# Performance work log

Hardware: AMD Instinct MI355X
Metric: run time of the kernel (lower is better)

The kernel has to match this reference:

```python
import jax, jax.numpy as jnp
import numpy as np

N = 4096
NUM_FEATURES = 1870
HIDDEN = 256
EMBED = 16
ALPHA = 0.2
NEG_BIG = -9e15
EPS = 1e-12


def setup_inputs() -> dict:
    key = jax.random.key(0)
    ks = jax.random.split(key, 9)
    x = jax.random.normal(ks[0], (N, NUM_FEATURES), dtype=jnp.float32)
    # sparse-ish binary adjacency mask (avg degree ~ 41) with self loops
    adj = (jax.random.uniform(ks[1], (N, N)) < 0.01).astype(jnp.float32)
    adj = jnp.maximum(adj, jnp.eye(N, dtype=jnp.float32))
    M = jax.random.uniform(ks[2], (N, N), dtype=jnp.float32)
    s1 = 1.0 / np.sqrt(NUM_FEATURES)
    s2 = 1.0 / np.sqrt(HIDDEN)
    W1 = jax.random.normal(ks[3], (NUM_FEATURES, HIDDEN), dtype=jnp.float32) * s1
    a_self1 = jax.random.normal(ks[4], (HIDDEN, 1), dtype=jnp.float32) * s2
    a_neighs1 = jax.random.normal(ks[5], (HIDDEN, 1), dtype=jnp.float32) * s2
    W2 = jax.random.normal(ks[6], (HIDDEN, EMBED), dtype=jnp.float32) * s2
    a_self2 = jax.random.normal(ks[7], (EMBED, 1), dtype=jnp.float32) / np.sqrt(EMBED)
    a_neighs2 = jax.random.normal(ks[8], (EMBED, 1), dtype=jnp.float32) / np.sqrt(EMBED)
    return {"x": x, "adj": adj, "M": M, "W1": W1, "a_self1": a_self1,
            "a_neighs1": a_neighs1, "W2": W2, "a_self2": a_self2, "a_neighs2": a_neighs2}


def gat_layer(x, adj, M, W, a_self, a_neighs, alpha):
    h = x @ W                                  # [N, out]
    f_self = h @ a_self                        # [N, 1]
    f_neigh = h @ a_neighs                     # [N, 1]
    e = jax.nn.leaky_relu((f_self + f_neigh.T) * M, negative_slope=alpha)  # [N, N]
    e = jnp.where(adj > 0, e, NEG_BIG)
    att = jax.nn.softmax(e, axis=1)            # row-stochastic over neighbors
    return jax.nn.elu(att @ h)                 # [N, out]


def reference(x, adj, M, W1, a_self1, a_neighs1, W2, a_self2, a_neighs2):
    h = gat_layer(x, adj, M, W1, a_self1, a_neighs1, ALPHA)
    h = gat_layer(h, adj, M, W2, a_self2, a_neighs2, ALPHA)
    # F.normalize(h, p=2, dim=1): divide by max(norm, eps)
    norm = jnp.maximum(jnp.linalg.norm(h, axis=1, keepdims=True), EPS)
    z = h / norm                               # [N, EMBED]
    A_pred = jax.nn.sigmoid(z @ z.T)           # [N, N]
    return (A_pred, z)
```

## Files before the change

kernel.cpp:

```cpp
#include <hip/hip_runtime.h>
#include <math.h>

#define NN 4096
#define NFEAT 1870
#define KPAD 2048
#define KSPLIT 8
#define KCHUNK 256
#define HID 256
#define EMB 16
#define MAXDEG 128

typedef __attribute__((ext_vector_type(8))) _Float16 f16x8;
typedef __attribute__((ext_vector_type(4))) float f32x4;

__device__ __forceinline__ ushort f2h(float f) {
    _Float16 h = (_Float16)f;
    return __builtin_bit_cast(ushort, h);
}

__global__ __launch_bounds__(256) void prep_kernel(
    const float* __restrict__ x, ushort* __restrict__ xf,
    const float* __restrict__ W1, ushort* __restrict__ Wh,
    const float* __restrict__ adj, const float* __restrict__ Mmat,
    int* __restrict__ nnz, int* __restrict__ gidx, float* __restrict__ Mg)
{
    const int b = blockIdx.x;
    const int tid = threadIdx.x;
    if (b < NN) {
        const int row = b;
        const int c0 = tid * 8;
        float v[8];
        if (c0 + 8 <= NFEAT) {
#pragma unroll
            for (int j = 0; j < 4; ++j) {
                float2 t = *(const float2*)&x[(size_t)row * NFEAT + c0 + j * 2];
                v[j * 2] = t.x; v[j * 2 + 1] = t.y;
            }
        } else {
#pragma unroll
            for (int j = 0; j < 8; ++j)
                v[j] = (c0 + j < NFEAT) ? x[(size_t)row * NFEAT + c0 + j] : 0.f;
        }
        ushort u[8];
#pragma unroll
        for (int j = 0; j < 8; ++j) u[j] = f2h(v[j]);
        *(int4*)&xf[(size_t)row * KPAD + c0] = *(int4*)u;
    } else if (b < NN + 128) {
        __shared__ float t[64][65];
        const int bb = b - NN;
        const int k0 = (bb & 31) * 64, n0 = (bb >> 5) * 64;
        const int kk = tid >> 2, c4 = (tid & 3) * 16;
#pragma unroll
        for (int j = 0; j < 4; ++j) {
            int k = k0 + kk;
            float4 v = make_float4(0.f, 0.f, 0.f, 0.f);
            if (k < NFEAT) v = *(const float4*)&W1[(size_t)k * HID + n0 + c4 + j * 4];
            t[kk][c4 + j * 4 + 0] = v.x; t[kk][c4 + j * 4 + 1] = v.y;
            t[kk][c4 + j * 4 + 2] = v.z; t[kk][c4 + j * 4 + 3] = v.w;
        }
        __syncthreads();
        const int on = tid >> 2, ok4 = (tid & 3) * 16;
#pragma unroll
        for (int j = 0; j < 4; ++j) {
            ushort hh[4];
#pragma unroll
            for (int i = 0; i < 4; ++i)
                hh[i] = f2h(t[ok4 + j * 4 + i][on]);
            size_t o = (size_t)(n0 + on) * KPAD + k0 + ok4 + j * 4;
            *(ushort4*)&Wh[o] = *(ushort4*)hh;
        }
    } else {
        __shared__ int sidx[4][MAXDEG];
        const int bb = b - NN - 128;
        const int wv = tid >> 6, lane = tid & 63;
        const int row = bb * 4 + wv;
        int base = 0;
#pragma unroll 4
        for (int t4 = 0; t4 < 16; ++t4) {
            int j0 = t4 * 256 + lane * 4;
            float4 a = *(const float4*)&adj[(size_t)row * NN + j0];
            float av[4] = {a.x, a.y, a.z, a.w};
#pragma unroll
            for (int c = 0; c < 4; ++c) {
                unsigned long long mb = __ballot(av[c] > 0.f);
                if (av[c] > 0.f) {
                    int pos = base + (int)__popcll(mb & ((1ull << lane) - 1ull));
                    if (pos < MAXDEG) sidx[wv][pos] = j0 + c;
                }
                base += (int)__popcll(mb);
            }
        }
        const int cnt = min(base, MAXDEG);
        if (lane == 0) nnz[row] = cnt;
        for (int s = lane; s < cnt; s += 64) {
            int j = sidx[wv][s];
            gidx[(size_t)row * MAXDEG + s] = j;
            Mg[(size_t)row * MAXDEG + s] = Mmat[(size_t)row * NN + j];
        }
    }
}

__global__ __launch_bounds__(256, 4) void gemm_xw1(
    const ushort* __restrict__ Ag,
    const ushort* __restrict__ Bg,
    float* __restrict__ Cpart)
{
    const int tid = threadIdx.x;
    const int lane = tid & 63;
    const int cgrp = tid >> 6;
    const int mgrp = blockIdx.x >> 3;
    const int z    = blockIdx.x & 7;
    const int row0 = mgrp * 32;
    const int col0 = cgrp * 64;
    const int kbeg = z * KCHUNK;

    const int fr = lane & 15, fs = lane >> 4;

    const ushort* Abase = Ag + (size_t)(row0 + fr) * KPAD + kbeg + fs * 8;
    const ushort* Bbase = Bg + (size_t)(col0 + fr) * KPAD + kbeg + fs * 8;

    f32x4 acc[2][4] = {};
#pragma unroll
    for (int sk = 0; sk < 8; ++sk) {
        f16x8 a[2], b[4];
#pragma unroll
        for (int m = 0; m < 2; ++m)
            a[m] = *(const f16x8*)&Abase[(size_t)m * 16 * KPAD + sk * 32];
#pragma unroll
        for (int n = 0; n < 4; ++n)
            b[n] = *(const f16x8*)&Bbase[(size_t)n * 16 * KPAD + sk * 32];
#pragma unroll
        for (int m = 0; m < 2; ++m)
#pragma unroll
            for (int n = 0; n < 4; ++n)
                acc[m][n] = __builtin_amdgcn_mfma_f32_16x16x32_f16(
                    a[m], b[n], acc[m][n], 0, 0, 0);
    }
    float* Cp = Cpart + (size_t)z * NN * HID;
#pragma unroll
    for (int m = 0; m < 2; ++m)
#pragma unroll
        for (int n = 0; n < 4; ++n)
#pragma unroll
            for (int r = 0; r < 4; ++r) {
                int row = row0 + m * 16 + fs * 4 + r;
                int col = col0 + n * 16 + fr;
                Cp[(size_t)row * HID + col] = acc[m][n][r];
            }
}

__global__ __launch_bounds__(256) void reduce_h1f_kernel(
    const float* __restrict__ part, float* __restrict__ h1,
    const float* __restrict__ a_s, const float* __restrict__ a_n,
    float* __restrict__ fs, float* __restrict__ fn)
{
    const int tid = threadIdx.x, wv = tid >> 6, lane = tid & 63;
    const int row = blockIdx.x * 4 + wv;
    const int d0 = lane * 4;
    const size_t o = (size_t)row * HID + d0;
    float4 s = *(const float4*)&part[o];
#pragma unroll
    for (int ch = 1; ch < KSPLIT; ++ch) {
        float4 p = *(const float4*)&part[(size_t)ch * NN * HID + o];
        s.x += p.x; s.y += p.y; s.z += p.z; s.w += p.w;
    }
    *(float4*)&h1[o] = s;
    float4 as4 = *(const float4*)&a_s[d0];
    float4 an4 = *(const float4*)&a_n[d0];
    float ps = s.x * as4.x + s.y * as4.y + s.z * as4.z + s.w * as4.w;
    float pn = s.x * an4.x + s.y * an4.y + s.z * an4.z + s.w * an4.w;
#pragma unroll
    for (int off = 32; off > 0; off >>= 1) {
        ps += __shfl_down(ps, off, 64);
        pn += __shfl_down(pn, off, 64);
    }
    if (lane == 0) { fs[row] = ps; fn[row] = pn; }
}

__global__ __launch_bounds__(256) void spmm1_kernel(
    const int* __restrict__ nnz, const int* __restrict__ gidx,
    const float* __restrict__ Mg,
    const float* __restrict__ fs, const float* __restrict__ fn,
    const float* __restrict__ h1, float* __restrict__ g1)
{
    __shared__ float p_s[MAXDEG];
    __shared__ int j_s[MAXDEG];
    __shared__ float wred[4], wsum[4];
    const int row = blockIdx.x;
    const int tid = threadIdx.x;
    const int lane = tid & 63, wv = tid >> 6;
    const int cnt = nnz[row];
    const float fsi = fs[row];

    float lmax = -3.0e38f;
    for (int s = tid; s < cnt; s += 256) {
        int j = gidx[(size_t)row * MAXDEG + s];
        j_s[s] = j;
        float e = (fsi + fn[j]) * Mg[(size_t)row * MAXDEG + s];
        e = (e > 0.f) ? e : 0.2f * e;
        p_s[s] = e;
        lmax = fmaxf(lmax, e);
    }
#pragma unroll
    for (int off = 32; off > 0; off >>= 1)
        lmax = fmaxf(lmax, __shfl_down(lmax, off, 64));
    if (lane == 0) wred[wv] = lmax;
    __syncthreads();
    const float m = fmaxf(fmaxf(wred[0], wred[1]), fmaxf(wred[2], wred[3]));

    float lsum = 0.f;
    for (int s = tid; s < cnt; s += 256) {
        float p = __expf(p_s[s] - m);
        p_s[s] = p;
        lsum += p;
    }
#pragma unroll
    for (int off = 32; off > 0; off >>= 1)
        lsum += __shfl_down(lsum, off, 64);
    if (lane == 0) wsum[wv] = lsum;
    __syncthreads();
    const float inv = 1.f / (wsum[0] + wsum[1] + wsum[2] + wsum[3]);

    float acc = 0.f;
#pragma unroll 4
    for (int s = 0; s < cnt; ++s)
        acc += p_s[s] * h1[(size_t)j_s[s] * HID + tid];
    float v = acc * inv;
    v = (v > 0.f) ? v : (__expf(v) - 1.f);
    g1[(size_t)row * HID + tid] = v;
}

__global__ __launch_bounds__(256) void gemm_h2_kernel(
    const float* __restrict__ g1, const float* __restrict__ W2,
    const float* __restrict__ a_s2, const float* __restrict__ a_n2,
    float* __restrict__ h2, float* __restrict__ fs2, float* __restrict__ fn2)
{
    __shared__ float Ws[256][16];
    __shared__ float Gs[16][257];
    const int tid = threadIdx.x;
    const int row0 = blockIdx.x * 16;
#pragma unroll
    for (int i = 0; i < 16; ++i) {
        int idx = tid + i * 256;
        Ws[idx >> 4][idx & 15] = W2[idx];
    }
#pragma unroll
    for (int i = 0; i < 16; ++i) {
        int idx = tid + i * 256;
        Gs[idx >> 8][idx & 255] = g1[(size_t)(row0 + (idx >> 8)) * HID + (idx & 255)];
    }
    __syncthreads();
    const int r = tid >> 4, c = tid & 15;
    float acc = 0.f;
#pragma unroll 8
    for (int k = 0; k < 256; ++k)
        acc += Gs[r][k] * Ws[k][c];
    h2[(size_t)(row0 + r) * EMB + c] = acc;

    float ps = acc * a_s2[c];
    float pn = acc * a_n2[c];
#pragma unroll
    for (int off = 1; off < 16; off <<= 1) {
        ps += __shfl_xor(ps, off, 64);
        pn += __shfl_xor(pn, off, 64);
    }
    if (c == 0) { fs2[row0 + r] = ps; fn2[row0 + r] = pn; }
}

__global__ __launch_bounds__(256) void spmm2_kernel(
    const int* __restrict__ nnz, const int* __restrict__ gidx,
    const float* __restrict__ Mg,
    const float* __restrict__ fs, const float* __restrict__ fn,
    const float* __restrict__ h2, float* __restrict__ z)
{
    __shared__ float p_s[4][MAXDEG];
    __shared__ int j_s[4][MAXDEG];
    const int tid = threadIdx.x;
    const int wv = tid >> 6, lane = tid & 63;
    const int row = blockIdx.x * 4 + wv;
    const int cnt = nnz[row];
    const float fsi = fs[row];

    float lmax = -3.0e38f;
    for (int s = lane; s < cnt; s += 64) {
        int j = gidx[(size_t)row * MAXDEG + s];
        j_s[wv][s] = j;
        float e = (fsi + fn[j]) * Mg[(size_t)row * MAXDEG + s];
        e = (e > 0.f) ? e : 0.2f * e;
        p_s[wv][s] = e;
        lmax = fmaxf(lmax, e);
    }
#pragma unroll
    for (int off = 1; off < 64; off <<= 1)
        lmax = fmaxf(lmax, __shfl_xor(lmax, off, 64));

    float lsum = 0.f;
    for (int s = lane; s < cnt; s += 64) {
        float p = __expf(p_s[wv][s] - lmax);
        p_s[wv][s] = p;
        lsum += p;
    }
#pragma unroll
    for (int off = 1; off < 64; off <<= 1)
        lsum += __shfl_xor(lsum, off, 64);
    const float inv = 1.f / lsum;

    const int s0 = lane >> 4, d = lane & 15;
    float acc = 0.f;
    for (int s = s0; s < cnt; s += 4)
        acc += p_s[wv][s] * h2[(size_t)j_s[wv][s] * EMB + d];
    acc += __shfl_xor(acc, 16, 64);
    acc += __shfl_xor(acc, 32, 64);

    float v = acc * inv;
    v = (v > 0.f) ? v : (__expf(v) - 1.f);
    float ss = v * v;
#pragma unroll
    for (int off = 1; off < 16; off <<= 1)
        ss += __shfl_xor(ss, off, 64);
    float zn = v / fmaxf(sqrtf(ss), 1e-12f);
    if (lane < 16) z[(size_t)row * EMB + lane] = zn;
}

__global__ __launch_bounds__(256) void apred_kernel(
    const float* __restrict__ z, float* __restrict__ out)
{
    __shared__ float zr[64][20];
    __shared__ float zc[64][20];
    const int tid = threadIdx.x;
    const int r0 = blockIdx.y * 64, c0 = blockIdx.x * 64;
#pragma unroll
    for (int i = 0; i < 4; ++i) {
        int idx = tid + i * 256;
        int rr = idx >> 4, d = idx & 15;
        zr[rr][d] = z[(size_t)(r0 + rr) * EMB + d];
        zc[rr][d] = z[(size_t)(c0 + rr) * EMB + d];
    }
    __syncthreads();
    const int tx = tid & 15, ty = tid >> 4;
    float rb[4][16], cb[4][16];
#pragma unroll
    for (int i = 0; i < 4; ++i)
#pragma unroll
        for (int d = 0; d < 16; ++d) {
            rb[i][d] = zr[ty * 4 + i][d];
            cb[i][d] = zc[tx * 4 + i][d];
        }
#pragma unroll
    for (int i = 0; i < 4; ++i) {
        float4 o;
        float v[4];
#pragma unroll
        for (int j = 0; j < 4; ++j) {
            float s = 0.f;
#pragma unroll
            for (int d = 0; d < 16; ++d) s += rb[i][d] * cb[j][d];
            v[j] = 1.f / (1.f + __expf(-s));
        }
        o.x = v[0]; o.y = v[1]; o.z = v[2]; o.w = v[3];
        *reinterpret_cast<float4*>(
            &out[(size_t)(r0 + ty * 4 + i) * NN + c0 + tx * 4]) = o;
    }
}

extern "C" void kernel_launch(void* const* d_in, const int* in_sizes, int n_in,
                              void* d_out, int out_size, void* d_ws, size_t ws_size,
                              hipStream_t stream)
{
    const float* x    = (const float*)d_in[0];
    const float* adj  = (const float*)d_in[1];
    const float* Mm   = (const float*)d_in[2];
    const float* W1   = (const float*)d_in[3];
    const float* a_s1 = (const float*)d_in[4];
    const float* a_n1 = (const float*)d_in[5];
    const float* W2   = (const float*)d_in[6];
    const float* a_s2 = (const float*)d_in[7];
    const float* a_n2 = (const float*)d_in[8];

    float* out = (float*)d_out;
    float* z   = out + (size_t)NN * NN;
    float* part = out;

    char* w = (char*)d_ws;
    float* h1    = (float*)w;  w += (size_t)NN * HID * 4;
    float* g1    = (float*)w;  w += (size_t)NN * HID * 4;
    ushort* xf16 = (ushort*)w; w += (size_t)NN * KPAD * 2;
    ushort* W1Th = (ushort*)w; w += (size_t)HID * KPAD * 2;
    float* h2    = (float*)w;  w += (size_t)NN * EMB * 4;
    int*   nnzp  = (int*)w;    w += NN * 4;
    int*   gidx  = (int*)w;    w += (size_t)NN * MAXDEG * 4;
    float* Mg    = (float*)w;  w += (size_t)NN * MAXDEG * 4;
    float* fs1   = (float*)w;  w += NN * 4;
    float* fn1   = (float*)w;  w += NN * 4;
    float* fs2   = (float*)w;  w += NN * 4;
    float* fn2   = (float*)w;  w += NN * 4;

    prep_kernel<<<NN + 128 + NN / 4, 256, 0, stream>>>(
        x, xf16, W1, W1Th, adj, Mm, nnzp, gidx, Mg);

    gemm_xw1<<<(NN / 32) * KSPLIT, 256, 0, stream>>>(xf16, W1Th, part);
    reduce_h1f_kernel<<<NN / 4, 256, 0, stream>>>(part, h1, a_s1, a_n1, fs1, fn1);
    spmm1_kernel<<<NN, 256, 0, stream>>>(nnzp, gidx, Mg, fs1, fn1, h1, g1);

    gemm_h2_kernel<<<256, 256, 0, stream>>>(g1, W2, a_s2, a_n2, h2, fs2, fn2);
    spmm2_kernel<<<NN / 4, 256, 0, stream>>>(nnzp, gidx, Mg, fs2, fn2, h2, z);

    apred_kernel<<<dim3(64, 64), 256, 0, stream>>>(z, out);
}
```

Measured before the change: 109.4 us.

## Fuse x fp16 conversion into GEMM and restructure adjacency compaction

The GEMM now reads fp32 x directly and converts it to fp16 in registers, which removes the separate x→fp16 pass and its staging buffer. K is padded only to 1920 with 4 splits of 480, and tiles are 16 rows per block. Loads for the next K step are issued before the current MFMAs run. Adjacency compaction now uses one block per row with a bitmask and a shuffle prefix scan instead of per-wave ballots. The cost is less register reuse of A per block and fp32 loads of x inside the GEMM.

```diff
diff --git a/kernel.cpp b/kernel.cpp
--- a/kernel.cpp
+++ b/kernel.cpp
@@ -3,9 +3,10 @@
 
 #define NN 4096
 #define NFEAT 1870
-#define KPAD 2048
-#define KSPLIT 8
-#define KCHUNK 256
+#define KB 1920
+#define KSPLIT 4
+#define KCHUNK 480
+#define NSTEP 15
 #define HID 256
 #define EMB 16
 #define MAXDEG 128
@@ -18,8 +19,34 @@
     return __builtin_bit_cast(ushort, h);
 }
 
+struct af32 { float2 v[4]; };
+
+__device__ __forceinline__ af32 load_a_raw(const float* __restrict__ rp, int k0) {
+    af32 r;
+    if (k0 + 8 <= NFEAT) {
+#pragma unroll
+        for (int j = 0; j < 4; ++j) r.v[j] = *(const float2*)&rp[k0 + j * 2];
+    } else {
+#pragma unroll
+        for (int j = 0; j < 4; ++j) {
+            float a = (k0 + j * 2     < NFEAT) ? rp[k0 + j * 2]     : 0.f;
+            float b = (k0 + j * 2 + 1 < NFEAT) ? rp[k0 + j * 2 + 1] : 0.f;
+            r.v[j] = make_float2(a, b);
+        }
+    }
+    return r;
+}
+__device__ __forceinline__ f16x8 cvt_a(af32 r) {
+    f16x8 o;
+#pragma unroll
+    for (int j = 0; j < 4; ++j) {
+        o[j * 2]     = (_Float16)r.v[j].x;
+        o[j * 2 + 1] = (_Float16)r.v[j].y;
+    }
+    return o;
+}
+
 __global__ __launch_bounds__(256) void prep_kernel(
-    const float* __restrict__ x, ushort* __restrict__ xf,
     const float* __restrict__ W1, ushort* __restrict__ Wh,
     const float* __restrict__ adj, const float* __restrict__ Mmat,
     int* __restrict__ nnz, int* __restrict__ gidx, float* __restrict__ Mg)
@@ -28,27 +55,53 @@
     const int tid = threadIdx.x;
     if (b < NN) {
         const int row = b;
-        const int c0 = tid * 8;
-        float v[8];
-        if (c0 + 8 <= NFEAT) {
-#pragma unroll
-            for (int j = 0; j < 4; ++j) {
-                float2 t = *(const float2*)&x[(size_t)row * NFEAT + c0 + j * 2];
-                v[j * 2] = t.x; v[j * 2 + 1] = t.y;
+        const int lane = tid & 63, wv = tid >> 6;
+        const float* arow = adj + (size_t)row * NN + tid * 16;
+        float4 v[4];
+#pragma unroll
+        for (int i = 0; i < 4; ++i) v[i] = *(const float4*)&arow[i * 4];
+        unsigned mask = 0;
+#pragma unroll
+        for (int i = 0; i < 4; ++i) {
+            if (v[i].x > 0.f) mask |= 1u << (i * 4 + 0);
+            if (v[i].y > 0.f) mask |= 1u << (i * 4 + 1);
+            if (v[i].z > 0.f) mask |= 1u << (i * 4 + 2);
+            if (v[i].w > 0.f) mask |= 1u << (i * 4 + 3);
+        }
+        const int cnt = __popc(mask);
+        int incl = cnt;
+#pragma unroll
+        for (int off = 1; off < 64; off <<= 1) {
+            int y = __shfl_up(incl, off, 64);
+            if (lane >= off) incl += y;
+        }
+        __shared__ int wsums[4];
+        if (lane == 63) wsums[wv] = incl;
+        __syncthreads();
+        int base = incl - cnt;
+#pragma unroll
+        for (int i = 0; i < 4; ++i)
+            if (i < wv) base += wsums[i];
+        if (tid == 0) {
+            int total = wsums[0] + wsums[1] + wsums[2] + wsums[3];
+            nnz[row] = min(total, MAXDEG);
+        }
+        unsigned mm = mask;
+        int off = base;
+        while (mm) {
+            int bit = __ffs(mm) - 1;
+            mm &= mm - 1;
+            if (off < MAXDEG) {
+                int j = tid * 16 + bit;
+                gidx[(size_t)row * MAXDEG + off] = j;
+                Mg[(size_t)row * MAXDEG + off] = Mmat[(size_t)row * NN + j];
             }
-        } else {
-#pragma unroll
-            for (int j = 0; j < 8; ++j)
-                v[j] = (c0 + j < NFEAT) ? x[(size_t)row * NFEAT + c0 + j] : 0.f;
-        }
-        ushort u[8];
-#pragma unroll
-        for (int j = 0; j < 8; ++j) u[j] = f2h(v[j]);
-        *(int4*)&xf[(size_t)row * KPAD + c0] = *(int4*)u;
-    } else if (b < NN + 128) {
+            ++off;
+        }
+    } else {
         __shared__ float t[64][65];
         const int bb = b - NN;
-        const int k0 = (bb & 31) * 64, n0 = (bb >> 5) * 64;
+        const int k0 = (bb % 30) * 64, n0 = (bb / 30) * 64;
         const int kk = tid >> 2, c4 = (tid & 3) * 16;
 #pragma unroll
         for (int j = 0; j < 4; ++j) {
@@ -66,87 +119,66 @@
 #pragma unroll
             for (int i = 0; i < 4; ++i)
                 hh[i] = f2h(t[ok4 + j * 4 + i][on]);
-            size_t o = (size_t)(n0 + on) * KPAD + k0 + ok4 + j * 4;
+            size_t o = (size_t)(n0 + on) * KB + k0 + ok4 + j * 4;
             *(ushort4*)&Wh[o] = *(ushort4*)hh;
         }
-    } else {
-        __shared__ int sidx[4][MAXDEG];
-        const int bb = b - NN - 128;
-        const int wv = tid >> 6, lane = tid & 63;
-        const int row = bb * 4 + wv;
-        int base = 0;
-#pragma unroll 4
-        for (int t4 = 0; t4 < 16; ++t4) {
-            int j0 = t4 * 256 + lane * 4;
-            float4 a = *(const float4*)&adj[(size_t)row * NN + j0];
-            float av[4] = {a.x, a.y, a.z, a.w};
-#pragma unroll
-            for (int c = 0; c < 4; ++c) {
-                unsigned long long mb = __ballot(av[c] > 0.f);
-                if (av[c] > 0.f) {
-                    int pos = base + (int)__popcll(mb & ((1ull << lane) - 1ull));
-                    if (pos < MAXDEG) sidx[wv][pos] = j0 + c;
-                }
-                base += (int)__popcll(mb);
-            }
-        }
-        const int cnt = min(base, MAXDEG);
-        if (lane == 0) nnz[row] = cnt;
-        for (int s = lane; s < cnt; s += 64) {
-            int j = sidx[wv][s];
-            gidx[(size_t)row * MAXDEG + s] = j;
-            Mg[(size_t)row * MAXDEG + s] = Mmat[(size_t)row * NN + j];
-        }
     }
 }
 
 __global__ __launch_bounds__(256, 4) void gemm_xw1(
-    const ushort* __restrict__ Ag,
+    const float* __restrict__ Xg,
     const ushort* __restrict__ Bg,
     float* __restrict__ Cpart)
 {
     const int tid = threadIdx.x;
     const int lane = tid & 63;
     const int cgrp = tid >> 6;
-    const int mgrp = blockIdx.x >> 3;
-    const int z    = blockIdx.x & 7;
-    const int row0 = mgrp * 32;
+    const int mgrp = blockIdx.x >> 2;
+    const int z    = blockIdx.x & 3;
+    const int row0 = mgrp * 16;
     const int col0 = cgrp * 64;
     const int kbeg = z * KCHUNK;
-
     const int fr = lane & 15, fs = lane >> 4;
 
-    const ushort* Abase = Ag + (size_t)(row0 + fr) * KPAD + kbeg + fs * 8;
-    const ushort* Bbase = Bg + (size_t)(col0 + fr) * KPAD + kbeg + fs * 8;
-
-    f32x4 acc[2][4] = {};
-#pragma unroll
-    for (int sk = 0; sk < 8; ++sk) {
-        f16x8 a[2], b[4];
-#pragma unroll
-        for (int m = 0; m < 2; ++m)
-            a[m] = *(const f16x8*)&Abase[(size_t)m * 16 * KPAD + sk * 32];
+    const float* Arow = Xg + (size_t)(row0 + fr) * NFEAT;
+    const ushort* Bbase = Bg + (size_t)(col0 + fr) * KB + kbeg + fs * 8;
+
+    af32 araw = load_a_raw(Arow, kbeg + fs * 8);
+    f16x8 bc[4];
+#pragma unroll
+    for (int n = 0; n < 4; ++n)
+        bc[n] = *(const f16x8*)&Bbase[(size_t)n * 16 * KB];
+
+    f32x4 acc[4] = {};
+#pragma unroll
+    for (int sk = 0; sk < NSTEP; ++sk) {
+        f16x8 ac = cvt_a(araw);
+        af32 anxt;
+        f16x8 bn[4];
+        if (sk + 1 < NSTEP) {
+            anxt = load_a_raw(Arow, kbeg + (sk + 1) * 32 + fs * 8);
+#pragma unroll
+            for (int n = 0; n < 4; ++n)
+                bn[n] = *(const f16x8*)&Bbase[(size_t)n * 16 * KB + (sk + 1) * 32];
+        }
 #pragma unroll
         for (int n = 0; n < 4; ++n)
-            b[n] = *(const f16x8*)&Bbase[(size_t)n * 16 * KPAD + sk * 32];
-#pragma unroll
-        for (int m = 0; m < 2; ++m)
-#pragma unroll
-            for (int n = 0; n < 4; ++n)
-                acc[m][n] = __builtin_amdgcn_mfma_f32_16x16x32_f16(
-                    a[m], b[n], acc[m][n], 0, 0, 0);
+            acc[n] = __builtin_amdgcn_mfma_f32_16x16x32_f16(ac, bc[n], acc[n], 0, 0, 0);
+        if (sk + 1 < NSTEP) {
+            araw = anxt;
+#pragma unroll
+            for (int n = 0; n < 4; ++n) bc[n] = bn[n];
+        }
     }
     float* Cp = Cpart + (size_t)z * NN * HID;
 #pragma unroll
-    for (int m = 0; m < 2; ++m)
-#pragma unroll
-        for (int n = 0; n < 4; ++n)
-#pragma unroll
-            for (int r = 0; r < 4; ++r) {
-                int row = row0 + m * 16 + fs * 4 + r;
-                int col = col0 + n * 16 + fr;
-                Cp[(size_t)row * HID + col] = acc[m][n][r];
-            }
+    for (int n = 0; n < 4; ++n)
+#pragma unroll
+        for (int r = 0; r < 4; ++r) {
+            int row = row0 + fs * 4 + r;
+            int col = col0 + n * 16 + fr;
+            Cp[(size_t)row * HID + col] = acc[n][r];
+        }
 }
 
 __global__ __launch_bounds__(256) void reduce_h1f_kernel(
@@ -384,8 +416,7 @@
     char* w = (char*)d_ws;
     float* h1    = (float*)w;  w += (size_t)NN * HID * 4;
     float* g1    = (float*)w;  w += (size_t)NN * HID * 4;
-    ushort* xf16 = (ushort*)w; w += (size_t)NN * KPAD * 2;
-    ushort* W1Th = (ushort*)w; w += (size_t)HID * KPAD * 2;
+    ushort* W1Th = (ushort*)w; w += (size_t)HID * KB * 2;
     float* h2    = (float*)w;  w += (size_t)NN * EMB * 4;
     int*   nnzp  = (int*)w;    w += NN * 4;
     int*   gidx  = (int*)w;    w += (size_t)NN * MAXDEG * 4;
@@ -395,10 +426,9 @@
     float* fs2   = (float*)w;  w += NN * 4;
     float* fn2   = (float*)w;  w += NN * 4;
 
-    prep_kernel<<<NN + 128 + NN / 4, 256, 0, stream>>>(
-        x, xf16, W1, W1Th, adj, Mm, nnzp, gidx, Mg);
-
-    gemm_xw1<<<(NN / 32) * KSPLIT, 256, 0, stream>>>(xf16, W1Th, part);
+    prep_kernel<<<NN + 120, 256, 0, stream>>>(W1, W1Th, adj, Mm, nnzp, gidx, Mg);
+
+    gemm_xw1<<<(NN / 16) * KSPLIT, 256, 0, stream>>>(x, W1Th, part);
     reduce_h1f_kernel<<<NN / 4, 256, 0, stream>>>(part, h1, a_s1, a_n1, fs1, fn1);
     spmm1_kernel<<<NN, 256, 0, stream>>>(nnzp, gidx, Mg, fs1, fn1, h1, g1);
 
```

Result: no change. 109.9 us (+0.4%).
